# Optimization experiments

Measured on AMD Instinct MI355X. Metric: run time of the kernel, lower is better.

Reference implementation:

```python
import jax, jax.numpy as jnp
import numpy as np

B, S, D = 2, 2048, 1024
H, HD = 16, 64  # H*HD == D (required by proj layer)
SCALE = D ** -0.5  # NOTE: original scales by full input dim (x.shape[-1]), not head dim


def setup_inputs() -> dict:
    key = jax.random.key(0)
    ks = jax.random.split(key, 7)
    std = D ** -0.5
    x = jax.random.normal(ks[0], (B, S, D), dtype=jnp.float32)
    # per-head projection weights, stacked: [H, D, HD] so x @ Wq[h] == Linear(D->HD)
    Wq = jax.random.normal(ks[1], (H, D, HD), dtype=jnp.float32) * std
    Wk = jax.random.normal(ks[2], (H, D, HD), dtype=jnp.float32) * std
    Wv = jax.random.normal(ks[3], (H, D, HD), dtype=jnp.float32) * std
    # output projection Linear(D, D) with bias
    Wp = jax.random.normal(ks[4], (D, D), dtype=jnp.float32) * std
    bp = jax.random.normal(ks[5], (D,), dtype=jnp.float32) * 0.01
    return {"x": x, "Wq": Wq, "Wk": Wk, "Wv": Wv, "Wp": Wp, "bp": bp}


def reference(x, Wq, Wk, Wv, Wp, bp):
    # All heads see the full x (atsp=False path). Dropout in eval mode (identity).
    q = jnp.einsum('bsd,hde->bhse', x, Wq)  # [B,H,S,HD]
    k = jnp.einsum('bsd,hde->bhse', x, Wk)
    v = jnp.einsum('bsd,hde->bhse', x, Wv)
    scores = jnp.einsum('bhse,bhte->bhst', q, k) * SCALE  # [B,H,S,S]
    causal = jnp.tril(jnp.ones((S, S), dtype=bool))
    scores = jnp.where(causal, scores, -jnp.inf)
    attn = jax.nn.softmax(scores, axis=-1)
    out = jnp.einsum('bhst,bhte->bhse', attn, v)          # [B,H,S,HD]
    # concat heads along last dim in head order: [B,S,H*HD]
    out = out.transpose(0, 2, 1, 3).reshape(B, S, H * HD)
    return out @ Wp.T + bp
```

## Files before the change

### kernel.cpp

```cpp
#include <hip/hip_runtime.h>

typedef __bf16 bf16x8 __attribute__((ext_vector_type(8)));
typedef __bf16 bf16x4 __attribute__((ext_vector_type(4)));
typedef float f32x4 __attribute__((ext_vector_type(4)));
typedef unsigned short u16;
typedef unsigned int u32;

static constexpr int kS = 2048, kD = 1024, kHD = 64;
static constexpr float kQScale = 0.03125f * 1.44269504f;

__device__ __forceinline__ u16 f2bf(float f) {
  union { float f; u32 u; } v; v.f = f;
  u32 r = v.u + 0x7FFFu + ((v.u >> 16) & 1u);
  return (u16)(r >> 16);
}
__device__ __forceinline__ float bf2f(u16 u) {
  union { u32 u; float f; } v; v.u = ((u32)u) << 16;
  return v.f;
}
__device__ __forceinline__ u32 pk2(float a, float b) {
  return (u32)f2bf(a) | ((u32)f2bf(b) << 16);
}
__device__ __forceinline__ f32x4 mfma16(bf16x8 a, bf16x8 b, f32x4 c) {
  return __builtin_amdgcn_mfma_f32_16x16x32_bf16(a, b, c, 0, 0, 0);
}
__device__ __forceinline__ void gld16(u16* lds, const u16* g) {
  __builtin_amdgcn_global_load_lds(
      (const __attribute__((address_space(1))) u32*)g,
      (__attribute__((address_space(3))) u32*)lds, 16, 0, 0);
}

__device__ __forceinline__ bool probe_f32(const u16* __restrict__ xr) {
  int ex = (xr[threadIdx.x] >> 7) & 0xFF;
  int n = __syncthreads_count(ex >= 134);
  return n > 8;
}

union Pack8 { u16 u[8]; uint4 v; };

__global__ void cast_all_kernel(const void* Wq, const void* Wk, const void* Wv,
                                const void* Wp, const void* x,
                                u16* __restrict__ Wt, u16* __restrict__ Wpb,
                                u16* __restrict__ xb) {
  bool f32m = probe_f32((const u16*)x);
  int bid = blockIdx.x;
  int t = threadIdx.x;
  __shared__ float Ts[64][65];
  if (bid < 768) {
    int u = bid >> 4;
    int d0 = (bid & 15) * 64;
    int w = u >> 4, h = u & 15;
    const void* srcv = (w == 0) ? Wq : (w == 1) ? Wk : Wv;
    const float* sf = (const float*)srcv + (size_t)h * kD * kHD;
    const u16*   sb = (const u16*)srcv + (size_t)h * kD * kHD;
    int row = t >> 4;
    int c4 = (t & 15) * 4;
    for (int rr = 0; rr < 64; rr += 16) {
      int r = rr + row;
      if (f32m) {
        float4 v = *(const float4*)&sf[(size_t)(d0 + r) * kHD + c4];
        Ts[r][c4 + 0] = v.x; Ts[r][c4 + 1] = v.y; Ts[r][c4 + 2] = v.z; Ts[r][c4 + 3] = v.w;
      } else {
        const u16* p = &sb[(size_t)(d0 + r) * kHD + c4];
        Ts[r][c4 + 0] = bf2f(p[0]); Ts[r][c4 + 1] = bf2f(p[1]);
        Ts[r][c4 + 2] = bf2f(p[2]); Ts[r][c4 + 3] = bf2f(p[3]);
      }
    }
    __syncthreads();
    for (int rr = 0; rr < 64; rr += 16) {
      int e = rr + row;
      uint2 pk;
      pk.x = pk2(Ts[c4 + 0][e], Ts[c4 + 1][e]);
      pk.y = pk2(Ts[c4 + 2][e], Ts[c4 + 3][e]);
      *(uint2*)&Wt[(size_t)u * (kHD * kD) + (size_t)e * kD + d0 + c4] = pk;
    }
  } else if (bid < 1792) {
    if (!f32m) return;
    int i = ((bid - 768) * 256 + t) * 4;
    float4 v = *(const float4*)((const float*)Wp + i);
    uint2 pk; pk.x = pk2(v.x, v.y); pk.y = pk2(v.z, v.w);
    *(uint2*)&Wpb[i] = pk;
  } else {
    if (!f32m) return;
    size_t i = ((size_t)(bid - 1792) * 256 + t) * 8;
    const float* xf = (const float*)x;
    float4 a = *(const float4*)&xf[i];
    float4 b = *(const float4*)&xf[i + 4];
    Pack8 pk;
    pk.u[0] = f2bf(a.x); pk.u[1] = f2bf(a.y); pk.u[2] = f2bf(a.z); pk.u[3] = f2bf(a.w);
    pk.u[4] = f2bf(b.x); pk.u[5] = f2bf(b.y); pk.u[6] = f2bf(b.z); pk.u[7] = f2bf(b.w);
    *(uint4*)&xb[i] = pk.v;
  }
}

__global__ __launch_bounds__(256) void qkv_gemm_kernel(const u16* __restrict__ xb,
    const u16* __restrict__ Wt, u16* __restrict__ Q, u16* __restrict__ K,
    u16* __restrict__ Vt, const void* __restrict__ x) {
  bool f32m = probe_f32((const u16*)x);
  const u16* xsrc = f32m ? xb : (const u16*)x;
  int m0 = blockIdx.x * 128;
  int n0 = blockIdx.y * 128;
  int w = (int)(blockIdx.y >> 3);
  const u16 *Ap, *Bp; int a0, b0;
  if (w == 2) { Ap = xsrc; a0 = m0; Bp = Wt; b0 = n0; }
  else        { Ap = Wt; a0 = n0; Bp = xsrc; b0 = m0; }
  int t = threadIdx.x;
  int wv = t >> 6, l = t & 63;
  int fr = l & 15, fq = l >> 4;
  int wI = (wv >> 1) * 64, wJ = (wv & 1) * 64;
  __shared__ __align__(16) u16 As[128][64];
  __shared__ __align__(16) u16 Bs[128][64];
  int srow = l >> 3;
  int scol = (((l & 7) ^ srow)) * 8;
  int dcol = (l & 7) * 8;
  int sw = fr & 7;
  f32x4 acc[4][4];
#pragma unroll
  for (int ii = 0; ii < 4; ++ii)
#pragma unroll
    for (int jj = 0; jj < 4; ++jj)
      for (int i = 0; i < 4; ++i) acc[ii][jj][i] = 0.f;

  for (int kb = 0; kb < kD / 64; ++kb) {
    int k0 = kb * 64;
    __syncthreads();
#pragma unroll
    for (int j = 0; j < 4; ++j) {
      int row = (wv * 4 + j) * 8 + srow;
      gld16(&As[row][dcol], &Ap[(size_t)(a0 + row) * kD + k0 + scol]);
      gld16(&Bs[row][dcol], &Bp[(size_t)(b0 + row) * kD + k0 + scol]);
    }
    __syncthreads();
    bf16x8 af[4][2], bg[4][2];
#pragma unroll
    for (int ii = 0; ii < 4; ++ii) {
      af[ii][0] = *(const bf16x8*)&As[wI + ii * 16 + fr][((0 + fq) ^ sw) * 8];
      af[ii][1] = *(const bf16x8*)&As[wI + ii * 16 + fr][((4 + fq) ^ sw) * 8];
    }
#pragma unroll
    for (int jj = 0; jj < 4; ++jj) {
      bg[jj][0] = *(const bf16x8*)&Bs[wJ + jj * 16 + fr][((0 + fq) ^ sw) * 8];
      bg[jj][1] = *(const bf16x8*)&Bs[wJ + jj * 16 + fr][((4 + fq) ^ sw) * 8];
    }
#pragma unroll
    for (int ii = 0; ii < 4; ++ii)
#pragma unroll
      for (int jj = 0; jj < 4; ++jj) {
        acc[ii][jj] = mfma16(af[ii][0], bg[jj][0], acc[ii][jj]);
        acc[ii][jj] = mfma16(af[ii][1], bg[jj][1], acc[ii][jj]);
      }
  }

  if (w == 2) {
    int uh = wv & 1;
    int u = 2 * blockIdx.y + uh;
    int h = u & 15;
#pragma unroll
    for (int jj = 0; jj < 4; ++jj) {
      int e = jj * 16 + fr;
#pragma unroll
      for (int ii = 0; ii < 4; ++ii) {
        int m = m0 + wI + ii * 16 + fq * 4;
        int b = m >> 11, s0 = m & 2047;
        int bh = b * 16 + h;
        *(bf16x4*)&Vt[((size_t)bh * kHD + e) * kS + s0] =
            __builtin_convertvector(acc[ii][jj], bf16x4);
      }
    }
  } else {
    int uh = wv >> 1;
    int u = 2 * blockIdx.y + uh;
    int h = u & 15;
    bool isQ = (w == 0);
    u16* dst = isQ ? Q : K;
#pragma unroll
    for (int jj = 0; jj < 4; ++jj) {
      int m = m0 + wJ + jj * 16 + fr;
      int b = m >> 11, s = m & 2047;
      int bh = b * 16 + h;
      size_t rowb = ((size_t)bh * kS + s) * kHD;
#pragma unroll
      for (int ii = 0; ii < 4; ++ii) {
        int e0 = ii * 16 + fq * 4;
        f32x4 v = acc[ii][jj];
        if (isQ) v *= kQScale;
        *(bf16x4*)&dst[rowb + e0] = __builtin_convertvector(v, bf16x4);
      }
    }
  }
}

__global__ __launch_bounds__(256) void attn_kernel(const u16* __restrict__ Q,
    const u16* __restrict__ K, const u16* __restrict__ Vt, u16* __restrict__ cat) {
  int qb = 31 - (int)(blockIdx.x >> 5);
  int bh = (int)(blockIdx.x & 31);
  int q0 = qb * 64;
  int t = threadIdx.x;
  int wv = t >> 6, l = t & 63;
  int fr = l & 15, fq = l >> 4;
  __shared__ __align__(16) u16 Ks[64][64];
  __shared__ __align__(16) u16 Vs[64][64];
  __shared__ __align__(16) u16 Ps[4][16][72];
  const u16* Qb = Q + (size_t)bh * kS * kHD;
  const u16* Kb = K + (size_t)bh * kS * kHD;
  const u16* Vb = Vt + (size_t)bh * kHD * kS;

  int qrow = q0 + wv * 16 + fr;
  bf16x8 qf0 = *(const bf16x8*)&Qb[(size_t)qrow * kHD + fq * 8];
  bf16x8 qf1 = *(const bf16x8*)&Qb[(size_t)qrow * kHD + 32 + fq * 8];

  f32x4 O[4];
#pragma unroll
  for (int nt = 0; nt < 4; ++nt) for (int i = 0; i < 4; ++i) O[nt][i] = 0.f;
  float lsum = 0.f;

  int srow0 = t >> 3, gcol = (t & 7) * 8;
  int srow1 = srow0 + 32;
  int scol = (((t & 7) ^ (srow0 & 7))) * 8;
  int sw = fr & 7;
  uint4 kr0 = *(const uint4*)&Kb[(size_t)srow0 * kHD + gcol];
  uint4 kr1 = *(const uint4*)&Kb[(size_t)srow1 * kHD + gcol];
  uint4 vr0 = *(const uint4*)&Vb[(size_t)srow0 * kS + gcol];
  uint4 vr1 = *(const uint4*)&Vb[(size_t)srow1 * kS + gcol];

  for (int tt = 0; tt <= qb; ++tt) {
    int t0 = tt * 64;
    __syncthreads();
    *(uint4*)&Ks[srow0][scol] = kr0;
    *(uint4*)&Ks[srow1][scol] = kr1;
    *(uint4*)&Vs[srow0][scol] = vr0;
    *(uint4*)&Vs[srow1][scol] = vr1;
    __syncthreads();
    if (tt < qb) {
      int t0n = t0 + 64;
      kr0 = *(const uint4*)&Kb[(size_t)(t0n + srow0) * kHD + gcol];
      kr1 = *(const uint4*)&Kb[(size_t)(t0n + srow1) * kHD + gcol];
      vr0 = *(const uint4*)&Vb[(size_t)srow0 * kS + t0n + gcol];
      vr1 = *(const uint4*)&Vb[(size_t)srow1 * kS + t0n + gcol];
    }
    f32x4 sc[4];
#pragma unroll
    for (int nt = 0; nt < 4; ++nt) {
      f32x4 z; z[0] = z[1] = z[2] = z[3] = 0.f;
      bf16x8 a0 = *(const bf16x8*)&Ks[nt * 16 + fr][((0 + fq) ^ sw) * 8];
      bf16x8 a1 = *(const bf16x8*)&Ks[nt * 16 + fr][((4 + fq) ^ sw) * 8];
      z = mfma16(a0, qf0, z);
      z = mfma16(a1, qf1, z);
      sc[nt] = z;
    }
    if (tt == qb) {
#pragma unroll
      for (int nt = 0; nt < 4; ++nt)
#pragma unroll
        for (int r = 0; r < 4; ++r)
          if (t0 + nt * 16 + fq * 4 + r > qrow) sc[nt][r] = -__builtin_inff();
    }
#pragma unroll
    for (int nt = 0; nt < 4; ++nt) {
#pragma unroll
      for (int r = 0; r < 4; ++r) {
        float p = exp2f(sc[nt][r]);
        sc[nt][r] = p;
        lsum += p;
      }
      *(bf16x4*)&Ps[wv][fr][nt * 16 + fq * 4] = __builtin_convertvector(sc[nt], bf16x4);
    }
    bf16x8 pf0 = *(const bf16x8*)&Ps[wv][fr][fq * 8];
    bf16x8 pf1 = *(const bf16x8*)&Ps[wv][fr][32 + fq * 8];
#pragma unroll
    for (int nt = 0; nt < 4; ++nt) {
      bf16x8 v0 = *(const bf16x8*)&Vs[nt * 16 + fr][((0 + fq) ^ sw) * 8];
      bf16x8 v1 = *(const bf16x8*)&Vs[nt * 16 + fr][((4 + fq) ^ sw) * 8];
      O[nt] = mfma16(v0, pf0, O[nt]);
      O[nt] = mfma16(v1, pf1, O[nt]);
    }
  }
  lsum += __shfl_xor(lsum, 16, 64);
  lsum += __shfl_xor(lsum, 32, 64);
  float inv = 1.0f / lsum;
  int b = bh >> 4, h = bh & 15;
  size_t rowbase = ((size_t)(b * kS + qrow)) * kD + h * kHD;
#pragma unroll
  for (int nt = 0; nt < 4; ++nt) {
    f32x4 ov = O[nt] * inv;
    *(bf16x4*)&cat[rowbase + nt * 16 + fq * 4] = __builtin_convertvector(ov, bf16x4);
  }
}

__global__ __launch_bounds__(256) void out_gemm_kernel(const u16* __restrict__ cat,
    const u16* __restrict__ Wpb, const void* __restrict__ Wp,
    const void* __restrict__ bp, void* __restrict__ out,
    const void* __restrict__ x) {
  bool f32m = probe_f32((const u16*)x);
  const u16* wsrc = f32m ? Wpb : (const u16*)Wp;
  int m0 = blockIdx.x * 64;
  int n0 = blockIdx.y * 128;
  int t = threadIdx.x;
  int wv = t >> 6, l = t & 63;
  int fr = l & 15, fq = l >> 4;
  int wI = (wv >> 1) * 64, wJ = (wv & 1) * 32;
  __shared__ __align__(16) u16 As[128][64];
  __shared__ __align__(16) u16 Bs[64][64];
  int srow = l >> 3;
  int scol = (((l & 7) ^ srow)) * 8;
  int dcol = (l & 7) * 8;
  int sw = fr & 7;
  f32x4 acc[4][2];
#pragma unroll
  for (int ii = 0; ii < 4; ++ii)
#pragma unroll
    for (int jj = 0; jj < 2; ++jj)
      for (int i = 0; i < 4; ++i) acc[ii][jj][i] = 0.f;

  for (int kb = 0; kb < kD / 64; ++kb) {
    int k0 = kb * 64;
    __syncthreads();
#pragma unroll
    for (int j = 0; j < 4; ++j) {
      int row = j * 32 + wv * 8 + srow;
      gld16(&As[row][dcol], &wsrc[(size_t)(n0 + row) * kD + k0 + scol]);
    }
#pragma unroll
    for (int j = 0; j < 2; ++j) {
      int row = j * 32 + wv * 8 + srow;
      gld16(&Bs[row][dcol], &cat[(size_t)(m0 + row) * kD + k0 + scol]);
    }
    __syncthreads();
    bf16x8 af[4][2], bg[2][2];
#pragma unroll
    for (int ii = 0; ii < 4; ++ii) {
      af[ii][0] = *(const bf16x8*)&As[wI + ii * 16 + fr][((0 + fq) ^ sw) * 8];
      af[ii][1] = *(const bf16x8*)&As[wI + ii * 16 + fr][((4 + fq) ^ sw) * 8];
    }
#pragma unroll
    for (int jj = 0; jj < 2; ++jj) {
      bg[jj][0] = *(const bf16x8*)&Bs[wJ + jj * 16 + fr][((0 + fq) ^ sw) * 8];
      bg[jj][1] = *(const bf16x8*)&Bs[wJ + jj * 16 + fr][((4 + fq) ^ sw) * 8];
    }
#pragma unroll
    for (int ii = 0; ii < 4; ++ii)
#pragma unroll
      for (int jj = 0; jj < 2; ++jj) {
        acc[ii][jj] = mfma16(af[ii][0], bg[jj][0], acc[ii][jj]);
        acc[ii][jj] = mfma16(af[ii][1], bg[jj][1], acc[ii][jj]);
      }
  }
  const float* bpf = (const float*)bp;
  const u16*   bpb = (const u16*)bp;
#pragma unroll
  for (int ii = 0; ii < 4; ++ii) {
    int n = n0 + wI + ii * 16 + fq * 4;
    f32x4 bias;
    if (f32m) bias = *(const f32x4*)&bpf[n];
    else { bias[0] = bf2f(bpb[n]); bias[1] = bf2f(bpb[n + 1]);
           bias[2] = bf2f(bpb[n + 2]); bias[3] = bf2f(bpb[n + 3]); }
#pragma unroll
    for (int jj = 0; jj < 2; ++jj) {
      int m = m0 + wJ + jj * 16 + fr;
      f32x4 v = acc[ii][jj] + bias;
      if (f32m) *(f32x4*)&((float*)out)[(size_t)m * kD + n] = v;
      else      *(bf16x4*)&((u16*)out)[(size_t)m * kD + n] = __builtin_convertvector(v, bf16x4);
    }
  }
}

extern "C" void kernel_launch(void* const* d_in, const int* in_sizes, int n_in,
                              void* d_out, int out_size, void* d_ws, size_t ws_size,
                              hipStream_t stream) {
  const void* x  = d_in[0];
  const void* Wq = d_in[1];
  const void* Wk = d_in[2];
  const void* Wv = d_in[3];
  const void* Wp = d_in[4];
  const void* bp = d_in[5];

  char* ws = (char*)d_ws;
  u16* Wt  = (u16*)(ws + 256);
  u16* Wpb = (u16*)(ws + 256 + 6291456);
  u16* Qp  = (u16*)(ws + 256 + 6291456 + 2097152);
  u16* Kp  = Qp  + (size_t)32 * 2048 * 64;
  u16* Vtp = Kp  + (size_t)32 * 2048 * 64;
  u16* xb  = Vtp + (size_t)32 * 2048 * 64;
  u16* cat = xb;

  cast_all_kernel<<<3840, 256, 0, stream>>>(Wq, Wk, Wv, Wp, x, Wt, Wpb, xb);
  qkv_gemm_kernel<<<dim3(32, 24), 256, 0, stream>>>(xb, Wt, Qp, Kp, Vtp, x);
  attn_kernel<<<1024, 256, 0, stream>>>(Qp, Kp, Vtp, cat);
  out_gemm_kernel<<<dim3(64, 8), 256, 0, stream>>>(cat, Wpb, Wp, bp, d_out, x);
}
```

Before: 171.2 us.

## Process 128 query rows per attention block to reuse K/V tiles

The attention kernel now assigns two 16-row query groups per wave, so each block covers 128 query rows instead of 64, and the grid is halved. Each K/V tile loaded into shared memory serves twice as many MFMAs, which cuts global and LDS traffic per query row. In exchange there are more registers per thread, lower occupancy, fewer blocks (512) for load balancing, and some extra masked work on the diagonal tiles.

Measured after the change: 183.9 us. +7.5%, slower.

```diff
diff --git a/kernel.cpp b/kernel.cpp
--- a/kernel.cpp
+++ b/kernel.cpp
@@ -192,27 +192,35 @@
 
 __global__ __launch_bounds__(256) void attn_kernel(const u16* __restrict__ Q,
     const u16* __restrict__ K, const u16* __restrict__ Vt, u16* __restrict__ cat) {
-  int qb = 31 - (int)(blockIdx.x >> 5);
+  int L = 15 - (int)(blockIdx.x >> 5);
   int bh = (int)(blockIdx.x & 31);
-  int q0 = qb * 64;
+  int q0 = L * 128;
   int t = threadIdx.x;
   int wv = t >> 6, l = t & 63;
   int fr = l & 15, fq = l >> 4;
   __shared__ __align__(16) u16 Ks[64][64];
   __shared__ __align__(16) u16 Vs[64][64];
-  __shared__ __align__(16) u16 Ps[4][16][72];
+  __shared__ __align__(16) u16 Ps[4][2][16][72];
   const u16* Qb = Q + (size_t)bh * kS * kHD;
   const u16* Kb = K + (size_t)bh * kS * kHD;
   const u16* Vb = Vt + (size_t)bh * kHD * kS;
 
-  int qrow = q0 + wv * 16 + fr;
-  bf16x8 qf0 = *(const bf16x8*)&Qb[(size_t)qrow * kHD + fq * 8];
-  bf16x8 qf1 = *(const bf16x8*)&Qb[(size_t)qrow * kHD + 32 + fq * 8];
-
-  f32x4 O[4];
-#pragma unroll
-  for (int nt = 0; nt < 4; ++nt) for (int i = 0; i < 4; ++i) O[nt][i] = 0.f;
-  float lsum = 0.f;
+  int qrow[2];
+  bf16x8 qf[2][2];
+#pragma unroll
+  for (int g = 0; g < 2; ++g) {
+    qrow[g] = q0 + wv * 32 + g * 16 + fr;
+    qf[g][0] = *(const bf16x8*)&Qb[(size_t)qrow[g] * kHD + fq * 8];
+    qf[g][1] = *(const bf16x8*)&Qb[(size_t)qrow[g] * kHD + 32 + fq * 8];
+  }
+
+  f32x4 O[2][4];
+#pragma unroll
+  for (int g = 0; g < 2; ++g)
+#pragma unroll
+    for (int nt = 0; nt < 4; ++nt)
+      for (int i = 0; i < 4; ++i) O[g][nt][i] = 0.f;
+  float lsum[2] = {0.f, 0.f};
 
   int srow0 = t >> 3, gcol = (t & 7) * 8;
   int srow1 = srow0 + 32;
@@ -223,7 +231,8 @@
   uint4 vr0 = *(const uint4*)&Vb[(size_t)srow0 * kS + gcol];
   uint4 vr1 = *(const uint4*)&Vb[(size_t)srow1 * kS + gcol];
 
-  for (int tt = 0; tt <= qb; ++tt) {
+  int ntile = 2 * L + 2;
+  for (int tt = 0; tt < ntile; ++tt) {
     int t0 = tt * 64;
     __syncthreads();
     *(uint4*)&Ks[srow0][scol] = kr0;
@@ -231,59 +240,78 @@
     *(uint4*)&Vs[srow0][scol] = vr0;
     *(uint4*)&Vs[srow1][scol] = vr1;
     __syncthreads();
-    if (tt < qb) {
+    if (tt + 1 < ntile) {
       int t0n = t0 + 64;
       kr0 = *(const uint4*)&Kb[(size_t)(t0n + srow0) * kHD + gcol];
       kr1 = *(const uint4*)&Kb[(size_t)(t0n + srow1) * kHD + gcol];
       vr0 = *(const uint4*)&Vb[(size_t)srow0 * kS + t0n + gcol];
       vr1 = *(const uint4*)&Vb[(size_t)srow1 * kS + t0n + gcol];
     }
-    f32x4 sc[4];
+    f32x4 sc[2][4];
 #pragma unroll
     for (int nt = 0; nt < 4; ++nt) {
-      f32x4 z; z[0] = z[1] = z[2] = z[3] = 0.f;
       bf16x8 a0 = *(const bf16x8*)&Ks[nt * 16 + fr][((0 + fq) ^ sw) * 8];
       bf16x8 a1 = *(const bf16x8*)&Ks[nt * 16 + fr][((4 + fq) ^ sw) * 8];
-      z = mfma16(a0, qf0, z);
-      z = mfma16(a1, qf1, z);
-      sc[nt] = z;
-    }
-    if (tt == qb) {
-#pragma unroll
-      for (int nt = 0; nt < 4; ++nt)
-#pragma unroll
-        for (int r = 0; r < 4; ++r)
-          if (t0 + nt * 16 + fq * 4 + r > qrow) sc[nt][r] = -__builtin_inff();
-    }
-#pragma unroll
-    for (int nt = 0; nt < 4; ++nt) {
-#pragma unroll
-      for (int r = 0; r < 4; ++r) {
-        float p = exp2f(sc[nt][r]);
-        sc[nt][r] = p;
-        lsum += p;
-      }
-      *(bf16x4*)&Ps[wv][fr][nt * 16 + fq * 4] = __builtin_convertvector(sc[nt], bf16x4);
-    }
-    bf16x8 pf0 = *(const bf16x8*)&Ps[wv][fr][fq * 8];
-    bf16x8 pf1 = *(const bf16x8*)&Ps[wv][fr][32 + fq * 8];
+#pragma unroll
+      for (int g = 0; g < 2; ++g) {
+        f32x4 z; z[0] = z[1] = z[2] = z[3] = 0.f;
+        z = mfma16(a0, qf[g][0], z);
+        z = mfma16(a1, qf[g][1], z);
+        sc[g][nt] = z;
+      }
+    }
+    if (tt >= 2 * L) {
+#pragma unroll
+      for (int g = 0; g < 2; ++g)
+#pragma unroll
+        for (int nt = 0; nt < 4; ++nt)
+#pragma unroll
+          for (int r = 0; r < 4; ++r)
+            if (t0 + nt * 16 + fq * 4 + r > qrow[g]) sc[g][nt][r] = -__builtin_inff();
+    }
+#pragma unroll
+    for (int g = 0; g < 2; ++g)
+#pragma unroll
+      for (int nt = 0; nt < 4; ++nt) {
+#pragma unroll
+        for (int r = 0; r < 4; ++r) {
+          float p = exp2f(sc[g][nt][r]);
+          sc[g][nt][r] = p;
+          lsum[g] += p;
+        }
+        *(bf16x4*)&Ps[wv][g][fr][nt * 16 + fq * 4] =
+            __builtin_convertvector(sc[g][nt], bf16x4);
+      }
+    bf16x8 pf[2][2];
+#pragma unroll
+    for (int g = 0; g < 2; ++g) {
+      pf[g][0] = *(const bf16x8*)&Ps[wv][g][fr][fq * 8];
+      pf[g][1] = *(const bf16x8*)&Ps[wv][g][fr][32 + fq * 8];
+    }
 #pragma unroll
     for (int nt = 0; nt < 4; ++nt) {
       bf16x8 v0 = *(const bf16x8*)&Vs[nt * 16 + fr][((0 + fq) ^ sw) * 8];
       bf16x8 v1 = *(const bf16x8*)&Vs[nt * 16 + fr][((4 + fq) ^ sw) * 8];
-      O[nt] = mfma16(v0, pf0, O[nt]);
-      O[nt] = mfma16(v1, pf1, O[nt]);
-    }
-  }
-  lsum += __shfl_xor(lsum, 16, 64);
-  lsum += __shfl_xor(lsum, 32, 64);
-  float inv = 1.0f / lsum;
+#pragma unroll
+      for (int g = 0; g < 2; ++g) {
+        O[g][nt] = mfma16(v0, pf[g][0], O[g][nt]);
+        O[g][nt] = mfma16(v1, pf[g][1], O[g][nt]);
+      }
+    }
+  }
   int b = bh >> 4, h = bh & 15;
-  size_t rowbase = ((size_t)(b * kS + qrow)) * kD + h * kHD;
-#pragma unroll
-  for (int nt = 0; nt < 4; ++nt) {
-    f32x4 ov = O[nt] * inv;
-    *(bf16x4*)&cat[rowbase + nt * 16 + fq * 4] = __builtin_convertvector(ov, bf16x4);
+#pragma unroll
+  for (int g = 0; g < 2; ++g) {
+    float s = lsum[g];
+    s += __shfl_xor(s, 16, 64);
+    s += __shfl_xor(s, 32, 64);
+    float inv = 1.0f / s;
+    size_t rowbase = ((size_t)(b * kS + qrow[g])) * kD + h * kHD;
+#pragma unroll
+    for (int nt = 0; nt < 4; ++nt) {
+      f32x4 ov = O[g][nt] * inv;
+      *(bf16x4*)&cat[rowbase + nt * 16 + fq * 4] = __builtin_convertvector(ov, bf16x4);
+    }
   }
 }
 
@@ -385,6 +413,6 @@
 
   cast_all_kernel<<<3840, 256, 0, stream>>>(Wq, Wk, Wv, Wp, x, Wt, Wpb, xb);
   qkv_gemm_kernel<<<dim3(32, 24), 256, 0, stream>>>(xb, Wt, Qp, Kp, Vtp, x);
-  attn_kernel<<<1024, 256, 0, stream>>>(Qp, Kp, Vtp, cat);
+  attn_kernel<<<512, 256, 0, stream>>>(Qp, Kp, Vtp, cat);
   out_gemm_kernel<<<dim3(64, 8), 256, 0, stream>>>(cat, Wpb, Wp, bp, d_out, x);
 }
```

## Double-buffer K/V tiles with direct global-to-LDS loads in attention kernel

Applied to the files above, without the earlier changes.

Replaces the register-staged K/V prefetch with direct global-to-LDS loads (gld16) into double-buffered shared tiles, so the next tile streams in while the current one is computed and one barrier per iteration is dropped. The swizzle moves from the LDS write side to the global read side. The P scratch buffer also switches from padded rows to an XOR swizzle, and s_setprio brackets around the MFMA sections raise wave priority during matrix work. This doubles K/V LDS use, which may lower occupancy, and it depends on gld16 semantics and on the wait before the barrier being correct.

New measurement: 173.1 us. About the same (+1.2%).

```diff
diff --git a/kernel.cpp b/kernel.cpp
--- a/kernel.cpp
+++ b/kernel.cpp
@@ -198,9 +198,9 @@
   int t = threadIdx.x;
   int wv = t >> 6, l = t & 63;
   int fr = l & 15, fq = l >> 4;
-  __shared__ __align__(16) u16 Ks[64][64];
-  __shared__ __align__(16) u16 Vs[64][64];
-  __shared__ __align__(16) u16 Ps[4][16][72];
+  __shared__ __align__(16) u16 Ks[2][64][64];
+  __shared__ __align__(16) u16 Vs[2][64][64];
+  __shared__ __align__(16) u16 Ps[4][16][64];
   const u16* Qb = Q + (size_t)bh * kS * kHD;
   const u16* Kb = K + (size_t)bh * kS * kHD;
   const u16* Vb = Vt + (size_t)bh * kHD * kS;
@@ -214,40 +214,41 @@
   for (int nt = 0; nt < 4; ++nt) for (int i = 0; i < 4; ++i) O[nt][i] = 0.f;
   float lsum = 0.f;
 
-  int srow0 = t >> 3, gcol = (t & 7) * 8;
-  int srow1 = srow0 + 32;
-  int scol = (((t & 7) ^ (srow0 & 7))) * 8;
+  int jr = l >> 3;
+  int dcol = (l & 7) * 8;
+  int scol = ((l & 7) ^ jr) * 8;
+  int r0 = wv * 16 + jr;
+  int r1 = r0 + 8;
   int sw = fr & 7;
-  uint4 kr0 = *(const uint4*)&Kb[(size_t)srow0 * kHD + gcol];
-  uint4 kr1 = *(const uint4*)&Kb[(size_t)srow1 * kHD + gcol];
-  uint4 vr0 = *(const uint4*)&Vb[(size_t)srow0 * kS + gcol];
-  uint4 vr1 = *(const uint4*)&Vb[(size_t)srow1 * kS + gcol];
-
+
+  gld16(&Ks[0][r0][dcol], &Kb[(size_t)r0 * kHD + scol]);
+  gld16(&Ks[0][r1][dcol], &Kb[(size_t)r1 * kHD + scol]);
+  gld16(&Vs[0][r0][dcol], &Vb[(size_t)r0 * kS + scol]);
+  gld16(&Vs[0][r1][dcol], &Vb[(size_t)r1 * kS + scol]);
+  __syncthreads();
+
+  int cur = 0;
   for (int tt = 0; tt <= qb; ++tt) {
     int t0 = tt * 64;
-    __syncthreads();
-    *(uint4*)&Ks[srow0][scol] = kr0;
-    *(uint4*)&Ks[srow1][scol] = kr1;
-    *(uint4*)&Vs[srow0][scol] = vr0;
-    *(uint4*)&Vs[srow1][scol] = vr1;
-    __syncthreads();
     if (tt < qb) {
       int t0n = t0 + 64;
-      kr0 = *(const uint4*)&Kb[(size_t)(t0n + srow0) * kHD + gcol];
-      kr1 = *(const uint4*)&Kb[(size_t)(t0n + srow1) * kHD + gcol];
-      vr0 = *(const uint4*)&Vb[(size_t)srow0 * kS + t0n + gcol];
-      vr1 = *(const uint4*)&Vb[(size_t)srow1 * kS + t0n + gcol];
+      gld16(&Ks[cur ^ 1][r0][dcol], &Kb[(size_t)(t0n + r0) * kHD + scol]);
+      gld16(&Ks[cur ^ 1][r1][dcol], &Kb[(size_t)(t0n + r1) * kHD + scol]);
+      gld16(&Vs[cur ^ 1][r0][dcol], &Vb[(size_t)r0 * kS + t0n + scol]);
+      gld16(&Vs[cur ^ 1][r1][dcol], &Vb[(size_t)r1 * kS + t0n + scol]);
     }
     f32x4 sc[4];
+    __builtin_amdgcn_s_setprio(1);
 #pragma unroll
     for (int nt = 0; nt < 4; ++nt) {
       f32x4 z; z[0] = z[1] = z[2] = z[3] = 0.f;
-      bf16x8 a0 = *(const bf16x8*)&Ks[nt * 16 + fr][((0 + fq) ^ sw) * 8];
-      bf16x8 a1 = *(const bf16x8*)&Ks[nt * 16 + fr][((4 + fq) ^ sw) * 8];
+      bf16x8 a0 = *(const bf16x8*)&Ks[cur][nt * 16 + fr][((0 + fq) ^ sw) * 8];
+      bf16x8 a1 = *(const bf16x8*)&Ks[cur][nt * 16 + fr][((4 + fq) ^ sw) * 8];
       z = mfma16(a0, qf0, z);
       z = mfma16(a1, qf1, z);
       sc[nt] = z;
     }
+    __builtin_amdgcn_s_setprio(0);
     if (tt == qb) {
 #pragma unroll
       for (int nt = 0; nt < 4; ++nt)
@@ -263,17 +264,22 @@
         sc[nt][r] = p;
         lsum += p;
       }
-      *(bf16x4*)&Ps[wv][fr][nt * 16 + fq * 4] = __builtin_convertvector(sc[nt], bf16x4);
-    }
-    bf16x8 pf0 = *(const bf16x8*)&Ps[wv][fr][fq * 8];
-    bf16x8 pf1 = *(const bf16x8*)&Ps[wv][fr][32 + fq * 8];
+      *(bf16x4*)&Ps[wv][fr][(((nt * 2 + (fq >> 1)) ^ sw) * 8) + (fq & 1) * 4] =
+          __builtin_convertvector(sc[nt], bf16x4);
+    }
+    bf16x8 pf0 = *(const bf16x8*)&Ps[wv][fr][(fq ^ sw) * 8];
+    bf16x8 pf1 = *(const bf16x8*)&Ps[wv][fr][((4 + fq) ^ sw) * 8];
+    __builtin_amdgcn_s_setprio(1);
 #pragma unroll
     for (int nt = 0; nt < 4; ++nt) {
-      bf16x8 v0 = *(const bf16x8*)&Vs[nt * 16 + fr][((0 + fq) ^ sw) * 8];
-      bf16x8 v1 = *(const bf16x8*)&Vs[nt * 16 + fr][((4 + fq) ^ sw) * 8];
+      bf16x8 v0 = *(const bf16x8*)&Vs[cur][nt * 16 + fr][((0 + fq) ^ sw) * 8];
+      bf16x8 v1 = *(const bf16x8*)&Vs[cur][nt * 16 + fr][((4 + fq) ^ sw) * 8];
       O[nt] = mfma16(v0, pf0, O[nt]);
       O[nt] = mfma16(v1, pf1, O[nt]);
     }
+    __builtin_amdgcn_s_setprio(0);
+    __syncthreads();
+    cur ^= 1;
   }
   lsum += __shfl_xor(lsum, 16, 64);
   lsum += __shfl_xor(lsum, 32, 64);
```
